# Performance work log

Hardware: AMD Instinct MI355X
Metric: run time of the kernel (lower is better)

The kernel has to match this reference:

```python
import jax, jax.numpy as jnp
import numpy as np

B, S, E, H = 2, 2048, 1024, 16
D = E // H  # head_dim = 64
SCALE = float(np.sqrt(D))


def setup_inputs() -> dict:
    root = jax.random.key(0)
    ks = jax.random.split(root, 12)
    inp = {
        "query": jax.random.normal(ks[0], (B, S, E), dtype=jnp.float32),
        "key": jax.random.normal(ks[1], (B, S, E), dtype=jnp.float32),
        "value": jax.random.normal(ks[2], (B, S, E), dtype=jnp.float32),
        "mask": jax.random.randint(ks[3], (B, S, S), 0, 2, dtype=jnp.int32),
        # Linear weights stored torch-style as [out, in]; init scale ~ 1/sqrt(E)
        "Wq": jax.random.normal(ks[4], (E, E), dtype=jnp.float32) / np.sqrt(E),
        "bq": jnp.zeros((E,), dtype=jnp.float32),
        "Wk": jax.random.normal(ks[5], (E, E), dtype=jnp.float32) / np.sqrt(E),
        "bk": jnp.zeros((E,), dtype=jnp.float32),
        "Wv": jax.random.normal(ks[6], (E, E), dtype=jnp.float32) / np.sqrt(E),
        "bv": jnp.zeros((E,), dtype=jnp.float32),
        "Wo": jax.random.normal(ks[7], (E, E), dtype=jnp.float32) / np.sqrt(E),
        "bo": jnp.zeros((E,), dtype=jnp.float32),
    }
    return inp


def reference(query, key, value, mask, Wq, bq, Wk, bk, Wv, bv, Wo, bo):
    # Projections (torch Linear: x @ W.T + b)
    Q = query @ Wq.T + bq
    K = key @ Wk.T + bk
    V = value @ Wv.T + bv
    # [B, S, E] -> [B, H, S, D]
    Q = Q.reshape(B, S, H, D).transpose(0, 2, 1, 3)
    K = K.reshape(B, S, H, D).transpose(0, 2, 1, 3)
    V = V.reshape(B, S, H, D).transpose(0, 2, 1, 3)
    # Scaled dot-product scores [B, H, S, S]
    scores = jnp.einsum("bhqd,bhkd->bhqk", Q, K) / SCALE
    # mask==0 positions -> -1e9 (mask broadcast over heads)
    scores = jnp.where(mask[:, None, :, :] == 0, jnp.float32(-1e9), scores)
    attn = jax.nn.softmax(scores, axis=-1)  # dropout is identity in eval
    out = jnp.einsum("bhqk,bhkd->bhqd", attn, V)
    out = out.transpose(0, 2, 1, 3).reshape(B, S, E)
    output = out @ Wo.T + bo
    avg_attn = attn.mean(axis=1)  # [B, S, S]
    return output, avg_attn
```

## Files before the change

### kernel.cpp

```cpp
#include <hip/hip_runtime.h>
#include <stdint.h>

#define BB 2
#define SS 2048
#define EE 1024
#define HH 16
#define DD 64
#define C1 0.18033688f
#define NT (SS / 64)

typedef _Float16 h16;
typedef _Float16 f16x8 __attribute__((ext_vector_type(8)));
typedef _Float16 f16x4 __attribute__((ext_vector_type(4)));
typedef float f32x4 __attribute__((ext_vector_type(4)));

#define SWZ(row, j) ((j) ^ ((row) & 7))

__device__ __forceinline__ void async_ld16(const void* g, void* l) {
  __builtin_amdgcn_global_load_lds((__attribute__((address_space(1))) void*)g,
                                   (__attribute__((address_space(3))) void*)l,
                                   16, 0, 0);
}

__global__ __launch_bounds__(256) void cvt_qkv(const float* __restrict__ q,
                                               const float* __restrict__ k,
                                               const float* __restrict__ v,
                                               h16* __restrict__ oq, h16* __restrict__ ok,
                                               h16* __restrict__ ov, int n4) {
  const float* s;
  h16* d;
  if (blockIdx.y == 0) { s = q; d = oq; }
  else if (blockIdx.y == 1) { s = k; d = ok; }
  else { s = v; d = ov; }
  int i = blockIdx.x * 256 + threadIdx.x;
  if (i >= n4) return;
  const float4 t = reinterpret_cast<const float4*>(s)[i];
  f16x4 o = {(_Float16)t.x, (_Float16)t.y, (_Float16)t.z, (_Float16)t.w};
  *reinterpret_cast<f16x4*>(d + i * 4) = o;
}

__global__ __launch_bounds__(256) void cvt_w4(const float* __restrict__ w0, const float* __restrict__ w1,
                                              const float* __restrict__ w2, const float* __restrict__ w3,
                                              h16* __restrict__ o0, h16* __restrict__ o1,
                                              h16* __restrict__ o2, h16* __restrict__ o3, int n4) {
  const float* s;
  h16* d;
  if (blockIdx.y == 0) { s = w0; d = o0; }
  else if (blockIdx.y == 1) { s = w1; d = o1; }
  else if (blockIdx.y == 2) { s = w2; d = o2; }
  else { s = w3; d = o3; }
  int i = blockIdx.x * 256 + threadIdx.x;
  if (i >= n4) return;
  const float4 t = reinterpret_cast<const float4*>(s)[i];
  f16x4 o = {(_Float16)t.x, (_Float16)t.y, (_Float16)t.z, (_Float16)t.w};
  *reinterpret_cast<f16x4*>(d + i * 4) = o;
}

__global__ __launch_bounds__(256) void pack_mask(const int* __restrict__ mask,
                                                 unsigned long long* __restrict__ pk) {
  const size_t i = (size_t)blockIdx.x * 256 + threadIdx.x;
  const unsigned long long b = __ballot(mask[i] != 0);
  if ((threadIdx.x & 63) == 0) pk[i >> 6] = b;
}

template <int MODE, bool SCALEQ>
__global__ __launch_bounds__(256, 4) void gemm_bt(const h16* __restrict__ A,
                                                  const h16* __restrict__ Bw,
                                                  const float* __restrict__ bias,
                                                  void* __restrict__ out) {
  constexpr int K = EE;
  __shared__ h16 As[2][64 * 64];
  __shared__ h16 Bs[2][64 * 64];
  const int tid = threadIdx.x;
  const int lane = tid & 63, w = tid >> 6;
  const int cg = lane & 15, rg = lane >> 4;
  const int wr = w >> 1, wc = w & 1;
  const int row0 = blockIdx.y * 64, col0 = blockIdx.x * 64;

  f32x4 acc[2][2] = {};

  const h16* Ag = A + (size_t)row0 * K;
  const h16* Bg = Bw + (size_t)col0 * K;

  auto stage = [&](int k0, int bi) {
#pragma unroll
    for (int i = 0; i < 2; ++i) {
      const int c = i * 256 + tid, row = c >> 3, jg = SWZ(row, c & 7);
      async_ld16(Ag + (size_t)row * K + k0 + jg * 8, (char*)As[bi] + c * 16);
      async_ld16(Bg + (size_t)row * K + k0 + jg * 8, (char*)Bs[bi] + c * 16);
    }
  };

  stage(0, 0);
  __syncthreads();
  for (int ks = 0; ks < K / 64; ++ks) {
    const int cur = ks & 1;
    if (ks + 1 < K / 64) stage((ks + 1) * 64, cur ^ 1);
#pragma unroll
    for (int kk = 0; kk < 2; ++kk) {
      f16x8 af[2], bfr[2];
#pragma unroll
      for (int m = 0; m < 2; ++m) {
        const int row = wr * 32 + m * 16 + cg;
        af[m] = *(const f16x8*)&As[cur][row * 64 + SWZ(row, kk * 4 + rg) * 8];
      }
#pragma unroll
      for (int n = 0; n < 2; ++n) {
        const int row = wc * 32 + n * 16 + cg;
        bfr[n] = *(const f16x8*)&Bs[cur][row * 64 + SWZ(row, kk * 4 + rg) * 8];
      }
#pragma unroll
      for (int m = 0; m < 2; ++m)
#pragma unroll
        for (int n = 0; n < 2; ++n)
          acc[m][n] = __builtin_amdgcn_mfma_f32_16x16x32_f16(af[m], bfr[n], acc[m][n], 0, 0, 0);
    }
    __syncthreads();
  }

#pragma unroll
  for (int n = 0; n < 2; ++n) {
    const int col = col0 + wc * 32 + n * 16 + cg;
    const float bv = bias[col];
#pragma unroll
    for (int m = 0; m < 2; ++m) {
#pragma unroll
      for (int j = 0; j < 4; ++j) {
        const int row = row0 + wr * 32 + m * 16 + rg * 4 + j;
        float v = acc[m][n][j] + bv;
        if (SCALEQ) v *= C1;
        if (MODE == 2) {
          ((float*)out)[(size_t)row * EE + col] = v;
        } else {
          const int b = row >> 11, s = row & (SS - 1);
          const int h = col >> 6, d = col & (DD - 1);
          size_t idx;
          if (MODE == 0) idx = (((size_t)b * HH + h) * SS + s) * DD + d;
          else           idx = (((size_t)b * HH + h) * DD + d) * SS + s;
          ((h16*)out)[idx] = (_Float16)v;
        }
      }
    }
  }
}

__global__ __launch_bounds__(512, 4) void attn_fwd(
    const h16* __restrict__ Qh, const h16* __restrict__ Kh, const h16* __restrict__ Vt,
    const uint2* __restrict__ mpk, h16* __restrict__ O, float* __restrict__ Crow) {
  __shared__ h16 Ks[2][64 * 64];
  __shared__ h16 Vs[2][64 * 64];
  __shared__ h16 Ps[8][16][72];
  const int tid = threadIdx.x;
  const int lane = tid & 63, w = tid >> 6;
  const int cg = lane & 15, rg = lane >> 4;
  const int qt = blockIdx.x, bh = blockIdx.y;
  const int b = bh >> 4, h = bh & (HH - 1);
  const int q0 = qt * 128 + w * 16;

  const h16* Qbase = Qh + ((size_t)bh * SS + q0 + cg) * DD;
  const f16x8 qf0 = *(const f16x8*)(Qbase + rg * 8);
  const f16x8 qf1 = *(const f16x8*)(Qbase + 32 + rg * 8);

  f32x4 o[4] = {};
  float mrun[4] = {-INFINITY, -INFINITY, -INFINITY, -INFINITY};
  float lrun[4] = {0.f, 0.f, 0.f, 0.f};

  const h16* Kg = Kh + (size_t)bh * SS * DD;
  const h16* Vg = Vt + (size_t)bh * DD * SS;
  const uint2* mb = mpk + ((size_t)b * SS + q0) * NT;

  auto stage = [&](int k0, int bi) {
    const int row = tid >> 3, jg = SWZ(row, tid & 7);
    async_ld16(Kg + (size_t)(k0 + row) * DD + jg * 8, (char*)Ks[bi] + tid * 16);
    async_ld16(Vg + (size_t)row * SS + k0 + jg * 8, (char*)Vs[bi] + tid * 16);
  };

  stage(0, 0);
  __syncthreads();
  for (int kt = 0; kt < NT; ++kt) {
    const int cur = kt & 1;
    if (kt + 1 < NT) stage((kt + 1) * 64, cur ^ 1);

    uint2 pk[4];
#pragma unroll
    for (int j = 0; j < 4; ++j) pk[j] = mb[(rg * 4 + j) * NT + kt];

    f32x4 sc[4];
#pragma unroll
    for (int n = 0; n < 4; ++n) {
      const int row = n * 16 + cg;
      const f16x8 kf0 = *(const f16x8*)&Ks[cur][row * 64 + SWZ(row, rg) * 8];
      const f16x8 kf1 = *(const f16x8*)&Ks[cur][row * 64 + SWZ(row, rg + 4) * 8];
      f32x4 z = {};
      z = __builtin_amdgcn_mfma_f32_16x16x32_f16(qf0, kf0, z, 0, 0, 0);
      sc[n] = __builtin_amdgcn_mfma_f32_16x16x32_f16(qf1, kf1, z, 0, 0, 0);
    }

    float tmv[4];
#pragma unroll
    for (int j = 0; j < 4; ++j) {
      float a = fmaxf(fmaxf(sc[0][j], sc[1][j]), fmaxf(sc[2][j], sc[3][j]));
      a = fmaxf(a, __shfl_xor(a, 1));
      a = fmaxf(a, __shfl_xor(a, 2));
      a = fmaxf(a, __shfl_xor(a, 4));
      a = fmaxf(a, __shfl_xor(a, 8));
      tmv[j] = a;
    }
    const float need = fmaxf(fmaxf(tmv[0] - mrun[0], tmv[1] - mrun[1]),
                             fmaxf(tmv[2] - mrun[2], tmv[3] - mrun[3]));
    if (!__all(need <= 8.0f)) {
#pragma unroll
      for (int j = 0; j < 4; ++j) {
        const float mn = fmaxf(mrun[j], tmv[j]);
        const float scl = exp2f(mrun[j] - mn);
        mrun[j] = mn;
        lrun[j] *= scl;
#pragma unroll
        for (int n = 0; n < 4; ++n) o[n][j] *= scl;
      }
    }
#pragma unroll
    for (int j = 0; j < 4; ++j) {
      float ps = 0.f;
#pragma unroll
      for (int n = 0; n < 4; ++n) {
        float p = exp2f(sc[n][j] - mrun[j]);
        const unsigned wb = (n & 2) ? pk[j].y : pk[j].x;
        p = ((wb >> ((n & 1) * 16 + cg)) & 1u) ? p : 0.f;
        ps += p;
        Ps[w][rg * 4 + j][n * 16 + cg] = (_Float16)p;
      }
      ps += __shfl_xor(ps, 1);
      ps += __shfl_xor(ps, 2);
      ps += __shfl_xor(ps, 4);
      ps += __shfl_xor(ps, 8);
      lrun[j] += ps;
    }

#pragma unroll
    for (int kkb = 0; kkb < 2; ++kkb) {
      const f16x8 pa = *(const f16x8*)&Ps[w][cg][kkb * 32 + rg * 8];
#pragma unroll
      for (int n = 0; n < 4; ++n) {
        const int row = n * 16 + cg;
        const f16x8 vf = *(const f16x8*)&Vs[cur][row * 64 + SWZ(row, kkb * 4 + rg) * 8];
        o[n] = __builtin_amdgcn_mfma_f32_16x16x32_f16(pa, vf, o[n], 0, 0, 0);
      }
    }
    __syncthreads();
  }

  float rl[4];
#pragma unroll
  for (int j = 0; j < 4; ++j) rl[j] = 1.f / lrun[j];
#pragma unroll
  for (int n = 0; n < 4; ++n)
#pragma unroll
    for (int j = 0; j < 4; ++j) {
      const int s = q0 + rg * 4 + j;
      O[((size_t)b * SS + s) * EE + h * DD + n * 16 + cg] = (_Float16)(o[n][j] * rl[j]);
    }
  if (cg == 0) {
#pragma unroll
    for (int j = 0; j < 4; ++j) {
      const int s = q0 + rg * 4 + j;
      Crow[(size_t)bh * SS + s] = mrun[j] + __log2f(lrun[j]);
    }
  }
}

__global__ __launch_bounds__(256, 4) void avg_attn_k(
    const h16* __restrict__ Qh, const h16* __restrict__ Kh,
    const uint2* __restrict__ mpk, const float* __restrict__ Crow,
    float* __restrict__ outAvg) {
  const int tid = threadIdx.x;
  const int lane = tid & 63, w = tid >> 6;
  const int cg = lane & 15, rg = lane >> 4;
  const int kt = blockIdx.x, qt = blockIdx.y, b = blockIdx.z;
  const int q0 = qt * 64 + w * 16, k0 = kt * 64;

  unsigned mbits = 0;
#pragma unroll
  for (int j = 0; j < 4; ++j) {
    const uint2 pk = mpk[((size_t)b * SS + q0 + rg * 4 + j) * NT + kt];
#pragma unroll
    for (int n = 0; n < 4; ++n) {
      const unsigned wbits = (n & 2) ? pk.y : pk.x;
      mbits |= ((wbits >> ((n & 1) * 16 + cg)) & 1u) << (j * 4 + n);
    }
  }

  f32x4 acc[4] = {};
#pragma unroll 2
  for (int h = 0; h < HH; ++h) {
    const int bh = b * HH + h;
    const h16* Qb = Qh + ((size_t)bh * SS + q0 + cg) * DD;
    const f16x8 qf0 = *(const f16x8*)(Qb + rg * 8);
    const f16x8 qf1 = *(const f16x8*)(Qb + 32 + rg * 8);
    const h16* Kb = Kh + ((size_t)bh * SS + k0) * DD;
    const float4 Cm = *(const float4*)(Crow + (size_t)bh * SS + q0 + rg * 4);
#pragma unroll
    for (int n = 0; n < 4; ++n) {
      const h16* kr = Kb + (size_t)(n * 16 + cg) * DD + rg * 8;
      const f16x8 kf0 = *(const f16x8*)kr;
      const f16x8 kf1 = *(const f16x8*)(kr + 32);
      f32x4 z = {};
      z = __builtin_amdgcn_mfma_f32_16x16x32_f16(qf0, kf0, z, 0, 0, 0);
      const f32x4 sc = __builtin_amdgcn_mfma_f32_16x16x32_f16(qf1, kf1, z, 0, 0, 0);
#pragma unroll
      for (int j = 0; j < 4; ++j) {
        const float cj = (j == 0) ? Cm.x : (j == 1) ? Cm.y : (j == 2) ? Cm.z : Cm.w;
        const float p = exp2f(sc[j] - cj);
        acc[n][j] += ((mbits >> (j * 4 + n)) & 1u) ? p : 0.f;
      }
    }
  }
#pragma unroll
  for (int n = 0; n < 4; ++n)
#pragma unroll
    for (int j = 0; j < 4; ++j)
      outAvg[((size_t)b * SS + q0 + rg * 4 + j) * SS + k0 + n * 16 + cg] = acc[n][j] * 0.0625f;
}

extern "C" void kernel_launch(void* const* d_in, const int* in_sizes, int n_in,
                              void* d_out, int out_size, void* d_ws, size_t ws_size,
                              hipStream_t stream) {
  const float* query = (const float*)d_in[0];
  const float* key_  = (const float*)d_in[1];
  const float* value = (const float*)d_in[2];
  const int*   mask  = (const int*)d_in[3];
  const float* Wq = (const float*)d_in[4];
  const float* bq = (const float*)d_in[5];
  const float* Wk = (const float*)d_in[6];
  const float* bk = (const float*)d_in[7];
  const float* Wv = (const float*)d_in[8];
  const float* bv = (const float*)d_in[9];
  const float* Wo = (const float*)d_in[10];
  const float* bo = (const float*)d_in[11];

  const size_t SZ_SE = (size_t)BB * SS * EE;
  h16* qx  = (h16*)d_ws;
  h16* kx  = qx + SZ_SE;
  h16* vx  = kx + SZ_SE;
  h16* wqx = vx + SZ_SE;
  h16* wkx = wqx + EE * EE;
  h16* wvx = wkx + EE * EE;
  h16* wox = wvx + EE * EE;
  h16* Qd  = wox + EE * EE;
  h16* Kd  = Qd + SZ_SE;
  h16* Vtd = Kd + SZ_SE;
  h16* Od  = Vtd + SZ_SE;
  float* Cr = (float*)(Od + SZ_SE);
  unsigned long long* mpk = (unsigned long long*)(Cr + (size_t)BB * HH * SS);

  float* outp = (float*)d_out;
  float* avgp = outp + SZ_SE;

  pack_mask<<<(BB * SS * SS) / 256, 256, 0, stream>>>(mask, mpk);
  cvt_qkv<<<dim3(4096, 3), 256, 0, stream>>>(query, key_, value, qx, kx, vx, (int)(SZ_SE / 4));
  cvt_w4<<<dim3(1024, 4), 256, 0, stream>>>(Wq, Wk, Wv, Wo, wqx, wkx, wvx, wox, EE * EE / 4);

  gemm_bt<0, true ><<<dim3(16, 64), 256, 0, stream>>>(qx, wqx, bq, Qd);
  gemm_bt<0, false><<<dim3(16, 64), 256, 0, stream>>>(kx, wkx, bk, Kd);
  gemm_bt<1, false><<<dim3(16, 64), 256, 0, stream>>>(vx, wvx, bv, Vtd);

  attn_fwd<<<dim3(SS / 128, BB * HH), 512, 0, stream>>>(Qd, Kd, Vtd, (const uint2*)mpk, Od, Cr);

  avg_attn_k<<<dim3(SS / 64, SS / 64, BB), 256, 0, stream>>>(Qd, Kd, (const uint2*)mpk, Cr, avgp);

  gemm_bt<2, false><<<dim3(16, 64), 256, 0, stream>>>(Od, wox, bo, outp);
}
```

Before: 495.1 us.

## Shrink attention blocks to 64 queries and process two key tiles per avg-attn block

attn_fwd now uses 256-thread blocks covering 64 query rows, with each thread staging two 16-byte chunks per K/V tile. This doubles the grid to 1024 blocks for better CU fill, at the cost of reloading K/V tiles twice as often per query. avg_attn_k now computes two adjacent 64-wide key tiles per block, reusing the Q fragments and the Crow loads across both and loading the mask as one uint4. That halves its grid and raises register pressure, and the unroll pragma on the head loop is dropped.

Measured after the change: 504.6 us. About the same (+1.9%).

```diff
diff --git a/kernel.cpp b/kernel.cpp
--- a/kernel.cpp
+++ b/kernel.cpp
@@ -144,18 +144,18 @@
   }
 }
 
-__global__ __launch_bounds__(512, 4) void attn_fwd(
+__global__ __launch_bounds__(256, 2) void attn_fwd(
     const h16* __restrict__ Qh, const h16* __restrict__ Kh, const h16* __restrict__ Vt,
     const uint2* __restrict__ mpk, h16* __restrict__ O, float* __restrict__ Crow) {
   __shared__ h16 Ks[2][64 * 64];
   __shared__ h16 Vs[2][64 * 64];
-  __shared__ h16 Ps[8][16][72];
+  __shared__ h16 Ps[4][16][72];
   const int tid = threadIdx.x;
   const int lane = tid & 63, w = tid >> 6;
   const int cg = lane & 15, rg = lane >> 4;
   const int qt = blockIdx.x, bh = blockIdx.y;
   const int b = bh >> 4, h = bh & (HH - 1);
-  const int q0 = qt * 128 + w * 16;
+  const int q0 = qt * 64 + w * 16;
 
   const h16* Qbase = Qh + ((size_t)bh * SS + q0 + cg) * DD;
   const f16x8 qf0 = *(const f16x8*)(Qbase + rg * 8);
@@ -170,9 +170,12 @@
   const uint2* mb = mpk + ((size_t)b * SS + q0) * NT;
 
   auto stage = [&](int k0, int bi) {
-    const int row = tid >> 3, jg = SWZ(row, tid & 7);
-    async_ld16(Kg + (size_t)(k0 + row) * DD + jg * 8, (char*)Ks[bi] + tid * 16);
-    async_ld16(Vg + (size_t)row * SS + k0 + jg * 8, (char*)Vs[bi] + tid * 16);
+#pragma unroll
+    for (int i = 0; i < 2; ++i) {
+      const int c = i * 256 + tid, row = c >> 3, jg = SWZ(row, c & 7);
+      async_ld16(Kg + (size_t)(k0 + row) * DD + jg * 8, (char*)Ks[bi] + c * 16);
+      async_ld16(Vg + (size_t)row * SS + k0 + jg * 8, (char*)Vs[bi] + c * 16);
+    }
   };
 
   stage(0, 0);
@@ -276,22 +279,23 @@
   const int tid = threadIdx.x;
   const int lane = tid & 63, w = tid >> 6;
   const int cg = lane & 15, rg = lane >> 4;
-  const int kt = blockIdx.x, qt = blockIdx.y, b = blockIdx.z;
+  const int kt = blockIdx.x * 2, qt = blockIdx.y, b = blockIdx.z;
   const int q0 = qt * 64 + w * 16, k0 = kt * 64;
 
-  unsigned mbits = 0;
+  unsigned mbA = 0, mbB = 0;
 #pragma unroll
   for (int j = 0; j < 4; ++j) {
-    const uint2 pk = mpk[((size_t)b * SS + q0 + rg * 4 + j) * NT + kt];
+    const uint4 pk = *(const uint4*)&mpk[((size_t)b * SS + q0 + rg * 4 + j) * NT + kt];
 #pragma unroll
     for (int n = 0; n < 4; ++n) {
-      const unsigned wbits = (n & 2) ? pk.y : pk.x;
-      mbits |= ((wbits >> ((n & 1) * 16 + cg)) & 1u) << (j * 4 + n);
-    }
-  }
-
-  f32x4 acc[4] = {};
-#pragma unroll 2
+      const unsigned wA = (n & 2) ? pk.y : pk.x;
+      const unsigned wB = (n & 2) ? pk.w : pk.z;
+      mbA |= ((wA >> ((n & 1) * 16 + cg)) & 1u) << (j * 4 + n);
+      mbB |= ((wB >> ((n & 1) * 16 + cg)) & 1u) << (j * 4 + n);
+    }
+  }
+
+  f32x4 accA[4] = {}, accB[4] = {};
   for (int h = 0; h < HH; ++h) {
     const int bh = b * HH + h;
     const h16* Qb = Qh + ((size_t)bh * SS + q0 + cg) * DD;
@@ -301,25 +305,35 @@
     const float4 Cm = *(const float4*)(Crow + (size_t)bh * SS + q0 + rg * 4);
 #pragma unroll
     for (int n = 0; n < 4; ++n) {
-      const h16* kr = Kb + (size_t)(n * 16 + cg) * DD + rg * 8;
-      const f16x8 kf0 = *(const f16x8*)kr;
-      const f16x8 kf1 = *(const f16x8*)(kr + 32);
-      f32x4 z = {};
-      z = __builtin_amdgcn_mfma_f32_16x16x32_f16(qf0, kf0, z, 0, 0, 0);
-      const f32x4 sc = __builtin_amdgcn_mfma_f32_16x16x32_f16(qf1, kf1, z, 0, 0, 0);
+      const h16* krA = Kb + (size_t)(n * 16 + cg) * DD + rg * 8;
+      const h16* krB = krA + 64 * DD;
+      const f16x8 kfA0 = *(const f16x8*)krA;
+      const f16x8 kfA1 = *(const f16x8*)(krA + 32);
+      const f16x8 kfB0 = *(const f16x8*)krB;
+      const f16x8 kfB1 = *(const f16x8*)(krB + 32);
+      f32x4 zA = {}, zB = {};
+      zA = __builtin_amdgcn_mfma_f32_16x16x32_f16(qf0, kfA0, zA, 0, 0, 0);
+      const f32x4 scA = __builtin_amdgcn_mfma_f32_16x16x32_f16(qf1, kfA1, zA, 0, 0, 0);
+      zB = __builtin_amdgcn_mfma_f32_16x16x32_f16(qf0, kfB0, zB, 0, 0, 0);
+      const f32x4 scB = __builtin_amdgcn_mfma_f32_16x16x32_f16(qf1, kfB1, zB, 0, 0, 0);
 #pragma unroll
       for (int j = 0; j < 4; ++j) {
         const float cj = (j == 0) ? Cm.x : (j == 1) ? Cm.y : (j == 2) ? Cm.z : Cm.w;
-        const float p = exp2f(sc[j] - cj);
-        acc[n][j] += ((mbits >> (j * 4 + n)) & 1u) ? p : 0.f;
+        const float pA = exp2f(scA[j] - cj);
+        const float pB = exp2f(scB[j] - cj);
+        accA[n][j] += ((mbA >> (j * 4 + n)) & 1u) ? pA : 0.f;
+        accB[n][j] += ((mbB >> (j * 4 + n)) & 1u) ? pB : 0.f;
       }
     }
   }
 #pragma unroll
   for (int n = 0; n < 4; ++n)
 #pragma unroll
-    for (int j = 0; j < 4; ++j)
-      outAvg[((size_t)b * SS + q0 + rg * 4 + j) * SS + k0 + n * 16 + cg] = acc[n][j] * 0.0625f;
+    for (int j = 0; j < 4; ++j) {
+      float* orow = outAvg + ((size_t)b * SS + q0 + rg * 4 + j) * SS + k0 + n * 16 + cg;
+      orow[0] = accA[n][j] * 0.0625f;
+      orow[64] = accB[n][j] * 0.0625f;
+    }
 }
 
 extern "C" void kernel_launch(void* const* d_in, const int* in_sizes, int n_in,
@@ -364,9 +378,9 @@
   gemm_bt<0, false><<<dim3(16, 64), 256, 0, stream>>>(kx, wkx, bk, Kd);
   gemm_bt<1, false><<<dim3(16, 64), 256, 0, stream>>>(vx, wvx, bv, Vtd);
 
-  attn_fwd<<<dim3(SS / 128, BB * HH), 512, 0, stream>>>(Qd, Kd, Vtd, (const uint2*)mpk, Od, Cr);
-
-  avg_attn_k<<<dim3(SS / 64, SS / 64, BB), 256, 0, stream>>>(Qd, Kd, (const uint2*)mpk, Cr, avgp);
+  attn_fwd<<<dim3(SS / 64, BB * HH), 256, 0, stream>>>(Qd, Kd, Vtd, (const uint2*)mpk, Od, Cr);
+
+  avg_attn_k<<<dim3(NT / 2, SS / 64, BB), 256, 0, stream>>>(Qd, Kd, (const uint2*)mpk, Cr, avgp);
 
   gemm_bt<2, false><<<dim3(16, 64), 256, 0, stream>>>(Od, wox, bo, outp);
 }
```
